# Kernel optimization log

Hardware: AMD Instinct MI355X
Metric: run time of the kernel (lower is better)

Reference implementation:

```python
import jax, jax.numpy as jnp
import numpy as np

SCALES = (2, 4, 8)  # primitive_scales, one per branch


def setup_inputs() -> dict:
    key = jax.random.key(0)
    k0, k1, k2, k3, k4 = jax.random.split(key, 5)
    B, C, H, W = 16, 256, 128, 128
    s = 1.0 / np.sqrt(C).astype(np.float32)
    return {
        "x": jax.random.normal(k0, (B, C, H, W), jnp.float32),
        "W_proto": jax.random.normal(k1, (3, C, C), jnp.float32) * s,
        "W_frame": jax.random.normal(k2, (3, C, C), jnp.float32) * s,
        "W_out": jax.random.normal(k3, (3, C, C), jnp.float32) * s,
        "W_fuse": jax.random.normal(k4, (C, 3 * C), jnp.float32) * (1.0 / np.sqrt(3 * C).astype(np.float32)),
    }


def _branch(x, Wp, Wf, Wo, P):
    # x: [B,C,H,W]; adaptive_avg_pool2d(x, (H, P)) with W % P == 0 == mean over equal bins along W
    B, C, H, W = x.shape
    proto = x.reshape(B, C, H, P, W // P).mean(axis=-1)        # [B,C,H,P]
    proto = jnp.einsum('oc,bchp->bohp', Wp, proto)             # proto_proj (1x1 conv)
    q = jnp.einsum('oc,bchw->bhwo', Wf, x)                     # frame_proj + permute -> [B,H,W,C]
    # att = q @ k, k = proto.permute(0,2,1,3) -> [B,H,C,P]
    att = jnp.einsum('bhwc,bchp->bhwp', q, proto) * (1.0 / jnp.sqrt(jnp.float32(C)))
    att = jax.nn.softmax(att, axis=-1)                         # [B,H,W,P]
    # v = proto.permute(0,2,3,1) -> [B,H,P,C]; msg = att @ v -> [B,H,W,C]
    msg = jnp.einsum('bhwp,bchp->bhwc', att, proto)
    return jnp.einsum('oc,bhwc->bohw', Wo, msg)                # out_proj -> [B,C,H,W]


def reference(x, W_proto, W_frame, W_out, W_fuse):
    outs = [_branch(x, W_proto[i], W_frame[i], W_out[i], SCALES[i]) for i in range(len(SCALES))]
    cat = jnp.concatenate(outs, axis=1)                        # [B, 3C, H, W]
    return jnp.einsum('oc,bchw->bohw', W_fuse, cat) + x
```

## Files before the change

kernel.cpp:

```cpp
#include <hip/hip_runtime.h>
#include <hip/hip_bf16.h>
#include <math.h>

#define CC   256
#define HW   (128*128)
#define MAT  (CC*CC)
#define NBH  2048
#define N0   4096
#define N1   8192
#define N2   16384

typedef __attribute__((ext_vector_type(8))) short bf16x8;
typedef __attribute__((ext_vector_type(4))) float f32x4;

__global__ __launch_bounds__(256) void k_mats1(
    const float* __restrict__ Wp, const float* __restrict__ Wf,
    const float* __restrict__ Wo, const float* __restrict__ Wfu,
    __hip_bfloat16* __restrict__ A, float* __restrict__ E)
{
    int idx = blockIdx.x;
    int t = threadIdx.x;
    if (idx < 3*CC) {
        int i = idx >> 8, c = idx & 255;
        const float* wf = Wf + (size_t)i*MAT;
        const float* wp = Wp + (size_t)i*MAT;
        float acc = 0.f;
        for (int o = 0; o < CC; ++o)
            acc += wf[o*CC + c] * wp[o*CC + t];
        A[(size_t)i*512*CC + (size_t)c*CC + t] = __float2bfloat16(acc);
    } else {
        idx -= 3*CC;
        int i = idx >> 8, o = idx & 255;
        const float* wo = Wo + (size_t)i*MAT;
        const float* wfu = Wfu + (size_t)o*(3*CC) + i*CC;
        float acc = 0.f;
        for (int c3 = 0; c3 < CC; ++c3)
            acc += wfu[c3] * wo[c3*CC + t];
        E[(size_t)i*MAT + (size_t)o*CC + t] = acc;
    }
}

__global__ __launch_bounds__(256) void k_mats2(
    const float* __restrict__ Wp, const float* __restrict__ E,
    __hip_bfloat16* __restrict__ A)
{
    int idx = blockIdx.x;
    int i = idx >> 8, o = idx & 255;
    int t = threadIdx.x;
    const float* e = E + (size_t)i*MAT + (size_t)o*CC;
    const float* wp = Wp + (size_t)i*MAT;
    float acc = 0.f;
    for (int c = 0; c < CC; ++c)
        acc += e[c] * wp[c*CC + t];
    A[(size_t)i*512*CC + (size_t)(256+o)*CC + t] = __float2bfloat16(acc);
}

__global__ __launch_bounds__(256) void k_poolA(
    const float* __restrict__ x, float* __restrict__ binsG)
{
    int bc = blockIdx.x;
    int t = threadIdx.x;
    const float4* xp = (const float4*)(x + (size_t)bc*HW) + t;
    __shared__ float bins[128][9];
    float4 v[16];
    #pragma unroll
    for (int i = 0; i < 16; ++i) v[i] = xp[i*256];
    int hb = t >> 5, bin = (t & 31) >> 2;
    #pragma unroll
    for (int i = 0; i < 16; ++i) {
        float s = v[i].x + v[i].y + v[i].z + v[i].w;
        s += __shfl_xor(s, 1);
        s += __shfl_xor(s, 2);
        if ((t & 3) == 0) bins[i*8 + hb][bin] = s;
    }
    __syncthreads();
    int h = t >> 1, b0 = (t & 1) * 4;
    float4 o;
    o.x = bins[h][b0+0]; o.y = bins[h][b0+1];
    o.z = bins[h][b0+2]; o.w = bins[h][b0+3];
    ((float4*)binsG)[(size_t)bc*256 + t] = o;
}

__global__ __launch_bounds__(256) void k_poolB(
    const float* __restrict__ binsG, __hip_bfloat16* __restrict__ Bt)
{
    int bh = blockIdx.x;
    int b = bh >> 7, h = bh & 127;
    int c = threadIdx.x;
    const float* g = binsG + (((size_t)b*256 + c)*128 + h)*8;
    float4 lo = *(const float4*)(g);
    float4 hi = *(const float4*)(g + 4);
    float b8[8] = {lo.x, lo.y, lo.z, lo.w, hi.x, hi.y, hi.z, hi.w};

    __hip_bfloat16* B0 = Bt;
    __hip_bfloat16* B1 = Bt + (size_t)N0*CC;
    __hip_bfloat16* B2 = Bt + (size_t)(N0+N1)*CC;
    B0[((size_t)bh*2 + 0)*CC + c] = __float2bfloat16((b8[0]+b8[1]+b8[2]+b8[3]) * (1.f/64.f));
    B0[((size_t)bh*2 + 1)*CC + c] = __float2bfloat16((b8[4]+b8[5]+b8[6]+b8[7]) * (1.f/64.f));
    #pragma unroll
    for (int j = 0; j < 4; ++j)
        B1[((size_t)bh*4 + j)*CC + c] = __float2bfloat16((b8[2*j]+b8[2*j+1]) * (1.f/32.f));
    #pragma unroll
    for (int j = 0; j < 8; ++j)
        B2[((size_t)bh*8 + j)*CC + c] = __float2bfloat16(b8[j] * (1.f/16.f));
}

__global__ __launch_bounds__(128) void k_gemm(
    const __hip_bfloat16* __restrict__ A,
    const __hip_bfloat16* __restrict__ Bt,
    float* __restrict__ Cc)
{
    int blk = blockIdx.x;
    int br, lb, LP, poff;
    if (blk < 256)      { br = 0; lb = blk;       LP = 1; poff = 0; }
    else if (blk < 768) { br = 1; lb = blk - 256; LP = 2; poff = 2; }
    else                { br = 2; lb = blk - 768; LP = 3; poff = 6; }
    size_t aoff  = (size_t)br*512*CC;
    size_t btoff = (br == 0) ? 0 : (br == 1 ? (size_t)N0*CC : (size_t)(N0+N1)*CC);
    const __hip_bfloat16* Ab = A  + aoff;
    const __hip_bfloat16* Bb = Bt + btoff;

    int rb = lb & 3, cb = lb >> 2;
    int wv = threadIdx.x >> 6, lane = threadIdx.x & 63;
    int row0 = rb*128 + wv*64;
    int col0 = cb*64;
    int lr = lane & 15, lk = (lane >> 4) * 8;

    f32x4 acc[4][4] = {};
    for (int kk = 0; kk < CC; kk += 32) {
        bf16x8 af[4], bfr[4];
        #pragma unroll
        for (int m = 0; m < 4; ++m)
            af[m] = *reinterpret_cast<const bf16x8*>(Ab + (size_t)(row0 + m*16 + lr)*CC + kk + lk);
        #pragma unroll
        for (int n = 0; n < 4; ++n)
            bfr[n] = *reinterpret_cast<const bf16x8*>(Bb + (size_t)(col0 + n*16 + lr)*CC + kk + lk);
        #pragma unroll
        for (int m = 0; m < 4; ++m)
            #pragma unroll
            for (int n = 0; n < 4; ++n)
                acc[m][n] = __builtin_amdgcn_mfma_f32_16x16x32_bf16(af[m], bfr[n], acc[m][n], 0, 0, 0);
    }

    int cr = (lane >> 4) * 4, ccol = lane & 15;
    int pm = (1 << LP) - 1;
    #pragma unroll
    for (int m = 0; m < 4; ++m) {
        #pragma unroll
        for (int n = 0; n < 4; ++n) {
            int colg = col0 + n*16 + ccol;
            int bh = colg >> LP, p = colg & pm;
            float* dst = Cc + (size_t)bh*8192 + poff + p;
            #pragma unroll
            for (int j = 0; j < 4; ++j) {
                int r = row0 + m*16 + cr + j;
                dst[r*16] = acc[m][n][j];
            }
        }
    }
}

template<int L>
__device__ __forceinline__ void softmax2(float2* a) {
    float mx = a[0].x, my = a[0].y;
    #pragma unroll
    for (int j = 1; j < L; ++j) { mx = fmaxf(mx, a[j].x); my = fmaxf(my, a[j].y); }
    float sx = 0.f, sy = 0.f;
    #pragma unroll
    for (int j = 0; j < L; ++j) {
        a[j].x = __expf(a[j].x - mx); sx += a[j].x;
        a[j].y = __expf(a[j].y - my); sy += a[j].y;
    }
    float rx = 1.f / sx, ry = 1.f / sy;
    #pragma unroll
    for (int j = 0; j < L; ++j) { a[j].x *= rx; a[j].y *= ry; }
}

__global__ __launch_bounds__(256) void k_main(
    const float* __restrict__ x, const float* __restrict__ Cc,
    float* __restrict__ out)
{
    int bh = blockIdx.x;
    int b = bh >> 7, h = bh & 127;
    int t = threadIdx.x;
    int lane = t & 63;
    int wv = __builtin_amdgcn_readfirstlane(t >> 6);
    const float* Cb = Cc + (size_t)bh * 8192;
    const float2* x2 = (const float2*)x + ((size_t)b*CC)*(HW/2) + h*64 + lane;
    float2*       o2 = (float2*)out     + ((size_t)b*CC)*(HW/2) + h*64 + lane;
    __shared__ float att_sx[2][64][15];
    __shared__ float att_sy[2][64][15];

    float2 att[14];
    #pragma unroll
    for (int p = 0; p < 14; ++p) att[p] = make_float2(0.f, 0.f);

    #pragma unroll 1
    for (int ccc = 0; ccc < 4; ++ccc) {
        float2 xv[16];
        #pragma unroll
        for (int j = 0; j < 16; ++j) {
            int c = ccc*64 + j*4 + wv;
            xv[j] = x2[c*(HW/2)];
        }
        #pragma unroll
        for (int j = 0; j < 16; ++j) {
            int c = ccc*64 + j*4 + wv;
            const float* mp = Cb + c*16;
            #pragma unroll
            for (int p = 0; p < 14; ++p) {
                att[p].x += xv[j].x * mp[p];
                att[p].y += xv[j].y * mp[p];
            }
        }
    }

    if (wv >= 2) {
        #pragma unroll
        for (int p = 0; p < 14; ++p) {
            att_sx[wv-2][lane][p] = att[p].x;
            att_sy[wv-2][lane][p] = att[p].y;
        }
    }
    __syncthreads();
    if (wv < 2) {
        #pragma unroll
        for (int p = 0; p < 14; ++p) {
            att[p].x += att_sx[wv][lane][p];
            att[p].y += att_sy[wv][lane][p];
        }
        if (wv == 1) {
            #pragma unroll
            for (int p = 0; p < 14; ++p) {
                att_sx[1][lane][p] = att[p].x;
                att_sy[1][lane][p] = att[p].y;
            }
        }
    }
    __syncthreads();
    if (wv == 0) {
        #pragma unroll
        for (int p = 0; p < 14; ++p) {
            att[p].x = (att[p].x + att_sx[1][lane][p]) * 0.0625f;
            att[p].y = (att[p].y + att_sy[1][lane][p]) * 0.0625f;
        }
        softmax2<2>(att + 0);
        softmax2<4>(att + 2);
        softmax2<8>(att + 6);
        #pragma unroll
        for (int p = 0; p < 14; ++p) {
            att_sx[0][lane][p] = att[p].x;
            att_sy[0][lane][p] = att[p].y;
        }
    }
    __syncthreads();
    #pragma unroll
    for (int p = 0; p < 14; ++p) {
        att[p].x = att_sx[0][lane][p];
        att[p].y = att_sy[0][lane][p];
    }

    #pragma unroll 1
    for (int ooo = 0; ooo < 4; ++ooo) {
        float2 xv[16];
        #pragma unroll
        for (int j = 0; j < 16; ++j) {
            int o = ooo*64 + j*4 + wv;
            xv[j] = x2[o*(HW/2)];
        }
        #pragma unroll
        for (int j = 0; j < 16; ++j) {
            int o = ooo*64 + j*4 + wv;
            const float* vp = Cb + (256 + o)*16;
            float2 acc = xv[j];
            #pragma unroll
            for (int p = 0; p < 14; ++p) {
                acc.x += att[p].x * vp[p];
                acc.y += att[p].y * vp[p];
            }
            o2[o*(HW/2)] = acc;
        }
    }
}

extern "C" void kernel_launch(void* const* d_in, const int* in_sizes, int n_in,
                              void* d_out, int out_size, void* d_ws, size_t ws_size,
                              hipStream_t stream)
{
    (void)in_sizes; (void)n_in; (void)out_size; (void)ws_size;
    const float* x   = (const float*)d_in[0];
    const float* Wp  = (const float*)d_in[1];
    const float* Wf  = (const float*)d_in[2];
    const float* Wo  = (const float*)d_in[3];
    const float* Wfu = (const float*)d_in[4];
    float* out = (float*)d_out;

    char* wsb = (char*)d_ws;
    float*          E     = (float*)wsb;
    __hip_bfloat16* A     = (__hip_bfloat16*)(wsb + 786432);
    __hip_bfloat16* Bt    = (__hip_bfloat16*)(wsb + 1572864);
    float*          Cc    = (float*)(wsb + 16252928);
    float*          binsG = Cc;

    k_mats1<<<dim3(6*CC),  dim3(256), 0, stream>>>(Wp, Wf, Wo, Wfu, A, E);
    k_mats2<<<dim3(3*CC),  dim3(256), 0, stream>>>(Wp, E, A);
    k_poolA<<<dim3(4096),  dim3(256), 0, stream>>>(x, binsG);
    k_poolB<<<dim3(NBH),   dim3(256), 0, stream>>>(binsG, Bt);
    k_gemm <<<dim3(1792),  dim3(128), 0, stream>>>(A, Bt, Cc);
    k_main <<<dim3(NBH),   dim3(256), 0, stream>>>(x, Cc, out);
}
```

Baseline: 347.8 us.

## Cache x slice in registers across both k_main passes; split pooling blocks in half

```diff
diff --git a/kernel.cpp b/kernel.cpp
--- a/kernel.cpp
+++ b/kernel.cpp
@@ -58,27 +58,30 @@
 __global__ __launch_bounds__(256) void k_poolA(
     const float* __restrict__ x, float* __restrict__ binsG)
 {
-    int bc = blockIdx.x;
+    int blk = blockIdx.x;
+    int bc = blk >> 1, half = blk & 1;
     int t = threadIdx.x;
-    const float4* xp = (const float4*)(x + (size_t)bc*HW) + t;
-    __shared__ float bins[128][9];
-    float4 v[16];
-    #pragma unroll
-    for (int i = 0; i < 16; ++i) v[i] = xp[i*256];
+    const float4* xp = (const float4*)(x + (size_t)bc*HW + half*8192) + t;
+    __shared__ float bins[64][9];
+    float4 v[8];
+    #pragma unroll
+    for (int i = 0; i < 8; ++i) v[i] = xp[i*256];
     int hb = t >> 5, bin = (t & 31) >> 2;
     #pragma unroll
-    for (int i = 0; i < 16; ++i) {
+    for (int i = 0; i < 8; ++i) {
         float s = v[i].x + v[i].y + v[i].z + v[i].w;
         s += __shfl_xor(s, 1);
         s += __shfl_xor(s, 2);
         if ((t & 3) == 0) bins[i*8 + hb][bin] = s;
     }
     __syncthreads();
-    int h = t >> 1, b0 = (t & 1) * 4;
-    float4 o;
-    o.x = bins[h][b0+0]; o.y = bins[h][b0+1];
-    o.z = bins[h][b0+2]; o.w = bins[h][b0+3];
-    ((float4*)binsG)[(size_t)bc*256 + t] = o;
+    if (t < 128) {
+        int h = t >> 1, b0 = (t & 1) * 4;
+        float4 o;
+        o.x = bins[h][b0+0]; o.y = bins[h][b0+1];
+        o.z = bins[h][b0+2]; o.w = bins[h][b0+3];
+        ((float4*)binsG)[(size_t)bc*256 + half*128 + t] = o;
+    }
 }
 
 __global__ __launch_bounds__(256) void k_poolB(
@@ -176,7 +179,7 @@
     for (int j = 0; j < L; ++j) { a[j].x *= rx; a[j].y *= ry; }
 }
 
-__global__ __launch_bounds__(256) void k_main(
+__global__ __launch_bounds__(256, 2) void k_main(
     const float* __restrict__ x, const float* __restrict__ Cc,
     float* __restrict__ out)
 {
@@ -191,27 +194,23 @@
     __shared__ float att_sx[2][64][15];
     __shared__ float att_sy[2][64][15];
 
+    float2 xc[64];
+    #pragma unroll
+    for (int j = 0; j < 64; ++j)
+        xc[j] = x2[(size_t)(j*4 + wv)*(HW/2)];
+
     float2 att[14];
     #pragma unroll
     for (int p = 0; p < 14; ++p) att[p] = make_float2(0.f, 0.f);
 
-    #pragma unroll 1
-    for (int ccc = 0; ccc < 4; ++ccc) {
-        float2 xv[16];
-        #pragma unroll
-        for (int j = 0; j < 16; ++j) {
-            int c = ccc*64 + j*4 + wv;
-            xv[j] = x2[c*(HW/2)];
-        }
-        #pragma unroll
-        for (int j = 0; j < 16; ++j) {
-            int c = ccc*64 + j*4 + wv;
-            const float* mp = Cb + c*16;
-            #pragma unroll
-            for (int p = 0; p < 14; ++p) {
-                att[p].x += xv[j].x * mp[p];
-                att[p].y += xv[j].y * mp[p];
-            }
+    #pragma unroll
+    for (int j = 0; j < 64; ++j) {
+        int c = j*4 + wv;
+        const float* mp = Cb + c*16;
+        #pragma unroll
+        for (int p = 0; p < 14; ++p) {
+            att[p].x += xc[j].x * mp[p];
+            att[p].y += xc[j].y * mp[p];
         }
     }
 
@@ -260,26 +259,17 @@
         att[p].y = att_sy[0][lane][p];
     }
 
-    #pragma unroll 1
-    for (int ooo = 0; ooo < 4; ++ooo) {
-        float2 xv[16];
-        #pragma unroll
-        for (int j = 0; j < 16; ++j) {
-            int o = ooo*64 + j*4 + wv;
-            xv[j] = x2[o*(HW/2)];
-        }
-        #pragma unroll
-        for (int j = 0; j < 16; ++j) {
-            int o = ooo*64 + j*4 + wv;
-            const float* vp = Cb + (256 + o)*16;
-            float2 acc = xv[j];
-            #pragma unroll
-            for (int p = 0; p < 14; ++p) {
-                acc.x += att[p].x * vp[p];
-                acc.y += att[p].y * vp[p];
-            }
-            o2[o*(HW/2)] = acc;
-        }
+    #pragma unroll
+    for (int j = 0; j < 64; ++j) {
+        int o = j*4 + wv;
+        const float* vp = Cb + (256 + o)*16;
+        float2 acc = xc[j];
+        #pragma unroll
+        for (int p = 0; p < 14; ++p) {
+            acc.x += att[p].x * vp[p];
+            acc.y += att[p].y * vp[p];
+        }
+        o2[(size_t)o*(HW/2)] = acc;
     }
 }
 
@@ -304,7 +294,7 @@
 
     k_mats1<<<dim3(6*CC),  dim3(256), 0, stream>>>(Wp, Wf, Wo, Wfu, A, E);
     k_mats2<<<dim3(3*CC),  dim3(256), 0, stream>>>(Wp, E, A);
-    k_poolA<<<dim3(4096),  dim3(256), 0, stream>>>(x, binsG);
+    k_poolA<<<dim3(8192),  dim3(256), 0, stream>>>(x, binsG);
     k_poolB<<<dim3(NBH),   dim3(256), 0, stream>>>(binsG, Bt);
     k_gemm <<<dim3(1792),  dim3(128), 0, stream>>>(A, Bt, Cc);
     k_main <<<dim3(NBH),   dim3(256), 0, stream>>>(x, Cc, out);
```

Result: slower. 491.7 us (+41.4%).

## Stage x through LDS with async triple buffering and store per-row matrices in bf16

Applied to the files above, without the earlier changes.

```diff
diff --git a/kernel.cpp b/kernel.cpp
--- a/kernel.cpp
+++ b/kernel.cpp
@@ -1,6 +1,7 @@
 #include <hip/hip_runtime.h>
 #include <hip/hip_bf16.h>
 #include <math.h>
+#include <stdint.h>
 
 #define CC   256
 #define HW   (128*128)
@@ -12,6 +13,8 @@
 
 typedef __attribute__((ext_vector_type(8))) short bf16x8;
 typedef __attribute__((ext_vector_type(4))) float f32x4;
+typedef __attribute__((address_space(3))) uint32_t lds_u32_t;
+typedef __attribute__((address_space(1))) const uint32_t glb_u32_t;
 
 __global__ __launch_bounds__(256) void k_mats1(
     const float* __restrict__ Wp, const float* __restrict__ Wf,
@@ -55,7 +58,7 @@
     A[(size_t)i*512*CC + (size_t)(256+o)*CC + t] = __float2bfloat16(acc);
 }
 
-__global__ __launch_bounds__(256) void k_poolA(
+__global__ __launch_bounds__(256, 4) void k_poolA(
     const float* __restrict__ x, float* __restrict__ binsG)
 {
     int bc = blockIdx.x;
@@ -108,7 +111,7 @@
 __global__ __launch_bounds__(128) void k_gemm(
     const __hip_bfloat16* __restrict__ A,
     const __hip_bfloat16* __restrict__ Bt,
-    float* __restrict__ Cc)
+    __hip_bfloat16* __restrict__ Cc)
 {
     int blk = blockIdx.x;
     int br, lb, LP, poff;
@@ -150,11 +153,11 @@
         for (int n = 0; n < 4; ++n) {
             int colg = col0 + n*16 + ccol;
             int bh = colg >> LP, p = colg & pm;
-            float* dst = Cc + (size_t)bh*8192 + poff + p;
+            __hip_bfloat16* dst = Cc + (size_t)bh*8192 + poff + p;
             #pragma unroll
             for (int j = 0; j < 4; ++j) {
                 int r = row0 + m*16 + cr + j;
-                dst[r*16] = acc[m][n][j];
+                dst[r*16] = __float2bfloat16(acc[m][n][j]);
             }
         }
     }
@@ -176,8 +179,8 @@
     for (int j = 0; j < L; ++j) { a[j].x *= rx; a[j].y *= ry; }
 }
 
-__global__ __launch_bounds__(256) void k_main(
-    const float* __restrict__ x, const float* __restrict__ Cc,
+__global__ __launch_bounds__(256, 4) void k_main(
+    const float* __restrict__ x, const __hip_bfloat16* __restrict__ Cc,
     float* __restrict__ out)
 {
     int bh = blockIdx.x;
@@ -185,9 +188,11 @@
     int t = threadIdx.x;
     int lane = t & 63;
     int wv = __builtin_amdgcn_readfirstlane(t >> 6);
-    const float* Cb = Cc + (size_t)bh * 8192;
-    const float2* x2 = (const float2*)x + ((size_t)b*CC)*(HW/2) + h*64 + lane;
-    float2*       o2 = (float2*)out     + ((size_t)b*CC)*(HW/2) + h*64 + lane;
+    const uint32_t* Cb = (const uint32_t*)(Cc + (size_t)bh*8192);
+    const float* xg = x  + ((size_t)b*CC)*HW + h*128;
+    float*       og = out + ((size_t)b*CC)*HW + h*128;
+
+    __shared__ float xbuf[3][32*128];
     __shared__ float att_sx[2][64][15];
     __shared__ float att_sy[2][64][15];
 
@@ -195,90 +200,123 @@
     #pragma unroll
     for (int p = 0; p < 14; ++p) att[p] = make_float2(0.f, 0.f);
 
+    auto STAGE = [&](int tt) {
+        int cb = (tt & 7) * 32;
+        float* bufp = xbuf[tt % 3];
+        #pragma unroll
+        for (int q = 0; q < 4; ++q) {
+            int c0 = cb + wv*8 + q*2;
+            const float* gp = xg + (size_t)(c0 + (lane >> 5))*HW + (lane & 31)*4;
+            float* lp = &bufp[(wv*8 + q*2)*128];
+            __builtin_amdgcn_global_load_lds((glb_u32_t*)gp, (lds_u32_t*)lp, 16, 0, 0);
+        }
+    };
+
+    STAGE(0);
+    STAGE(1);
+
     #pragma unroll 1
-    for (int ccc = 0; ccc < 4; ++ccc) {
-        float2 xv[16];
-        #pragma unroll
-        for (int j = 0; j < 16; ++j) {
-            int c = ccc*64 + j*4 + wv;
-            xv[j] = x2[c*(HW/2)];
-        }
-        #pragma unroll
-        for (int j = 0; j < 16; ++j) {
-            int c = ccc*64 + j*4 + wv;
-            const float* mp = Cb + c*16;
+    for (int tt = 0; tt < 16; ++tt) {
+        if (tt < 15) asm volatile("s_waitcnt vmcnt(4)" ::: "memory");
+        else         asm volatile("s_waitcnt vmcnt(0)" ::: "memory");
+        __builtin_amdgcn_s_barrier();
+        __builtin_amdgcn_sched_barrier(0);
+
+        if (tt == 8) {
+            if (wv >= 2) {
+                #pragma unroll
+                for (int p = 0; p < 14; ++p) {
+                    att_sx[wv-2][lane][p] = att[p].x;
+                    att_sy[wv-2][lane][p] = att[p].y;
+                }
+            }
+            asm volatile("s_waitcnt lgkmcnt(0)" ::: "memory");
+            __builtin_amdgcn_s_barrier();
+            __builtin_amdgcn_sched_barrier(0);
+            if (wv < 2) {
+                #pragma unroll
+                for (int p = 0; p < 14; ++p) {
+                    att[p].x += att_sx[wv][lane][p];
+                    att[p].y += att_sy[wv][lane][p];
+                }
+                if (wv == 1) {
+                    #pragma unroll
+                    for (int p = 0; p < 14; ++p) {
+                        att_sx[1][lane][p] = att[p].x;
+                        att_sy[1][lane][p] = att[p].y;
+                    }
+                }
+            }
+            asm volatile("s_waitcnt lgkmcnt(0)" ::: "memory");
+            __builtin_amdgcn_s_barrier();
+            __builtin_amdgcn_sched_barrier(0);
+            if (wv == 0) {
+                #pragma unroll
+                for (int p = 0; p < 14; ++p) {
+                    att[p].x = (att[p].x + att_sx[1][lane][p]) * 0.0625f;
+                    att[p].y = (att[p].y + att_sy[1][lane][p]) * 0.0625f;
+                }
+                softmax2<2>(att + 0);
+                softmax2<4>(att + 2);
+                softmax2<8>(att + 6);
+                #pragma unroll
+                for (int p = 0; p < 14; ++p) {
+                    att_sx[0][lane][p] = att[p].x;
+                    att_sy[0][lane][p] = att[p].y;
+                }
+            }
+            asm volatile("s_waitcnt lgkmcnt(0)" ::: "memory");
+            __builtin_amdgcn_s_barrier();
+            __builtin_amdgcn_sched_barrier(0);
             #pragma unroll
             for (int p = 0; p < 14; ++p) {
-                att[p].x += xv[j].x * mp[p];
-                att[p].y += xv[j].y * mp[p];
+                att[p].x = att_sx[0][lane][p];
+                att[p].y = att_sy[0][lane][p];
             }
         }
-    }
-
-    if (wv >= 2) {
-        #pragma unroll
-        for (int p = 0; p < 14; ++p) {
-            att_sx[wv-2][lane][p] = att[p].x;
-            att_sy[wv-2][lane][p] = att[p].y;
-        }
-    }
-    __syncthreads();
-    if (wv < 2) {
-        #pragma unroll
-        for (int p = 0; p < 14; ++p) {
-            att[p].x += att_sx[wv][lane][p];
-            att[p].y += att_sy[wv][lane][p];
-        }
-        if (wv == 1) {
+
+        if (tt + 2 < 16) STAGE(tt + 2);
+
+        {
+            int cb = (tt & 7) * 32;
+            bool passB = (tt >= 8);
+            const float* xb = &xbuf[tt % 3][(wv*8)*128];
+            int crow = (passB ? 256 : 0) + cb + wv*8;
+            const uint32_t* wr = Cb + (size_t)crow*8;
             #pragma unroll
-            for (int p = 0; p < 14; ++p) {
-                att_sx[1][lane][p] = att[p].x;
-                att_sy[1][lane][p] = att[p].y;
-            }
-        }
-    }
-    __syncthreads();
-    if (wv == 0) {
-        #pragma unroll
-        for (int p = 0; p < 14; ++p) {
-            att[p].x = (att[p].x + att_sx[1][lane][p]) * 0.0625f;
-            att[p].y = (att[p].y + att_sy[1][lane][p]) * 0.0625f;
-        }
-        softmax2<2>(att + 0);
-        softmax2<4>(att + 2);
-        softmax2<8>(att + 6);
-        #pragma unroll
-        for (int p = 0; p < 14; ++p) {
-            att_sx[0][lane][p] = att[p].x;
-            att_sy[0][lane][p] = att[p].y;
-        }
-    }
-    __syncthreads();
-    #pragma unroll
-    for (int p = 0; p < 14; ++p) {
-        att[p].x = att_sx[0][lane][p];
-        att[p].y = att_sy[0][lane][p];
-    }
-
-    #pragma unroll 1
-    for (int ooo = 0; ooo < 4; ++ooo) {
-        float2 xv[16];
-        #pragma unroll
-        for (int j = 0; j < 16; ++j) {
-            int o = ooo*64 + j*4 + wv;
-            xv[j] = x2[o*(HW/2)];
-        }
-        #pragma unroll
-        for (int j = 0; j < 16; ++j) {
-            int o = ooo*64 + j*4 + wv;
-            const float* vp = Cb + (256 + o)*16;
-            float2 acc = xv[j];
-            #pragma unroll
-            for (int p = 0; p < 14; ++p) {
-                acc.x += att[p].x * vp[p];
-                acc.y += att[p].y * vp[p];
-            }
-            o2[o*(HW/2)] = acc;
+            for (int half = 0; half < 2; ++half) {
+                uint32_t u[4][7];
+                #pragma unroll
+                for (int q = 0; q < 4; ++q)
+                    #pragma unroll
+                    for (int j = 0; j < 7; ++j)
+                        u[q][j] = wr[(half*4 + q)*8 + j];
+                #pragma unroll
+                for (int q = 0; q < 4; ++q) {
+                    int qq = half*4 + q;
+                    float2 xv = *(const float2*)&xb[qq*128 + lane*2];
+                    if (!passB) {
+                        #pragma unroll
+                        for (int j = 0; j < 7; ++j) {
+                            float mlo = __uint_as_float(u[q][j] << 16);
+                            float mhi = __uint_as_float(u[q][j] & 0xFFFF0000u);
+                            att[2*j].x   += xv.x * mlo;  att[2*j].y   += xv.y * mlo;
+                            att[2*j+1].x += xv.x * mhi;  att[2*j+1].y += xv.y * mhi;
+                        }
+                    } else {
+                        float2 acc = xv;
+                        #pragma unroll
+                        for (int j = 0; j < 7; ++j) {
+                            float vlo = __uint_as_float(u[q][j] << 16);
+                            float vhi = __uint_as_float(u[q][j] & 0xFFFF0000u);
+                            acc.x += att[2*j].x * vlo;   acc.y += att[2*j].y * vlo;
+                            acc.x += att[2*j+1].x * vhi; acc.y += att[2*j+1].y * vhi;
+                        }
+                        int o = cb + wv*8 + qq;
+                        *(float2*)&og[(size_t)o*HW + lane*2] = acc;
+                    }
+                }
+            }
         }
     }
 }
@@ -299,8 +337,8 @@
     float*          E     = (float*)wsb;
     __hip_bfloat16* A     = (__hip_bfloat16*)(wsb + 786432);
     __hip_bfloat16* Bt    = (__hip_bfloat16*)(wsb + 1572864);
-    float*          Cc    = (float*)(wsb + 16252928);
-    float*          binsG = Cc;
+    __hip_bfloat16* Cc    = (__hip_bfloat16*)(wsb + 16252928);
+    float*          binsG = (float*)(wsb + 16252928);
 
     k_mats1<<<dim3(6*CC),  dim3(256), 0, stream>>>(Wp, Wf, Wo, Wfu, A, E);
     k_mats2<<<dim3(3*CC),  dim3(256), 0, stream>>>(Wp, E, A);
```

Measured after the change: 334.1 us. 4.0% less time.

## Store per-row coefficient table in bf16 and double-buffer x loads in k_main

Applied to the files above, without the earlier changes.

```diff
diff --git a/kernel.cpp b/kernel.cpp
--- a/kernel.cpp
+++ b/kernel.cpp
@@ -1,6 +1,7 @@
 #include <hip/hip_runtime.h>
 #include <hip/hip_bf16.h>
 #include <math.h>
+#include <stdint.h>
 
 #define CC   256
 #define HW   (128*128)
@@ -55,7 +56,7 @@
     A[(size_t)i*512*CC + (size_t)(256+o)*CC + t] = __float2bfloat16(acc);
 }
 
-__global__ __launch_bounds__(256) void k_poolA(
+__global__ __launch_bounds__(256, 4) void k_poolA(
     const float* __restrict__ x, float* __restrict__ binsG)
 {
     int bc = blockIdx.x;
@@ -108,7 +109,7 @@
 __global__ __launch_bounds__(128) void k_gemm(
     const __hip_bfloat16* __restrict__ A,
     const __hip_bfloat16* __restrict__ Bt,
-    float* __restrict__ Cc)
+    __hip_bfloat16* __restrict__ Cc)
 {
     int blk = blockIdx.x;
     int br, lb, LP, poff;
@@ -150,11 +151,11 @@
         for (int n = 0; n < 4; ++n) {
             int colg = col0 + n*16 + ccol;
             int bh = colg >> LP, p = colg & pm;
-            float* dst = Cc + (size_t)bh*8192 + poff + p;
+            __hip_bfloat16* dst = Cc + (size_t)bh*8192 + poff + p;
             #pragma unroll
             for (int j = 0; j < 4; ++j) {
                 int r = row0 + m*16 + cr + j;
-                dst[r*16] = acc[m][n][j];
+                dst[r*16] = __float2bfloat16(acc[m][n][j]);
             }
         }
     }
@@ -176,8 +177,8 @@
     for (int j = 0; j < L; ++j) { a[j].x *= rx; a[j].y *= ry; }
 }
 
-__global__ __launch_bounds__(256) void k_main(
-    const float* __restrict__ x, const float* __restrict__ Cc,
+__global__ __launch_bounds__(256, 4) void k_main(
+    const float* __restrict__ x, const __hip_bfloat16* __restrict__ Cc,
     float* __restrict__ out)
 {
     int bh = blockIdx.x;
@@ -185,7 +186,7 @@
     int t = threadIdx.x;
     int lane = t & 63;
     int wv = __builtin_amdgcn_readfirstlane(t >> 6);
-    const float* Cb = Cc + (size_t)bh * 8192;
+    const uint32_t* Cb = (const uint32_t*)(Cc + (size_t)bh*8192);
     const float2* x2 = (const float2*)x + ((size_t)b*CC)*(HW/2) + h*64 + lane;
     float2*       o2 = (float2*)out     + ((size_t)b*CC)*(HW/2) + h*64 + lane;
     __shared__ float att_sx[2][64][15];
@@ -195,25 +196,59 @@
     #pragma unroll
     for (int p = 0; p < 14; ++p) att[p] = make_float2(0.f, 0.f);
 
-    #pragma unroll 1
-    for (int ccc = 0; ccc < 4; ++ccc) {
-        float2 xv[16];
-        #pragma unroll
-        for (int j = 0; j < 16; ++j) {
-            int c = ccc*64 + j*4 + wv;
-            xv[j] = x2[c*(HW/2)];
-        }
-        #pragma unroll
-        for (int j = 0; j < 16; ++j) {
-            int c = ccc*64 + j*4 + wv;
-            const float* mp = Cb + c*16;
-            #pragma unroll
-            for (int p = 0; p < 14; ++p) {
-                att[p].x += xv[j].x * mp[p];
-                att[p].y += xv[j].y * mp[p];
-            }
-        }
-    }
+    float2 xa[8], xb[8];
+
+    #define CH(cc, j) (((cc)*8 + (j))*4 + wv)
+
+    #define LOADB(buf, cc)                                                  \
+        _Pragma("unroll")                                                   \
+        for (int j = 0; j < 8; ++j)                                         \
+            buf[j] = x2[(size_t)CH(cc, j) * (HW/2)];
+
+    #define CONS_A(buf, cc)                                                 \
+        _Pragma("unroll")                                                   \
+        for (int j = 0; j < 8; ++j) {                                       \
+            int c = CH(cc, j);                                              \
+            const uint32_t* wr = Cb + (size_t)c*8;                          \
+            float2 xv = buf[j];                                             \
+            _Pragma("unroll")                                               \
+            for (int p = 0; p < 7; ++p) {                                   \
+                uint32_t u = wr[p];                                         \
+                float mlo = __uint_as_float(u << 16);                       \
+                float mhi = __uint_as_float(u & 0xFFFF0000u);               \
+                att[2*p].x   += xv.x * mlo;  att[2*p].y   += xv.y * mlo;    \
+                att[2*p+1].x += xv.x * mhi;  att[2*p+1].y += xv.y * mhi;    \
+            }                                                               \
+        }
+
+    #define CONS_B(buf, cc)                                                 \
+        _Pragma("unroll")                                                   \
+        for (int j = 0; j < 8; ++j) {                                       \
+            int c = CH(cc, j);                                              \
+            const uint32_t* wr = Cb + (size_t)(256 + c)*8;                  \
+            float2 acc = buf[j];                                            \
+            _Pragma("unroll")                                               \
+            for (int p = 0; p < 7; ++p) {                                   \
+                uint32_t u = wr[p];                                         \
+                float vlo = __uint_as_float(u << 16);                       \
+                float vhi = __uint_as_float(u & 0xFFFF0000u);               \
+                acc.x += att[2*p].x * vlo;   acc.y += att[2*p].y * vlo;     \
+                acc.x += att[2*p+1].x * vhi; acc.y += att[2*p+1].y * vhi;   \
+            }                                                               \
+            o2[(size_t)c * (HW/2)] = acc;                                   \
+        }
+
+    #define SB __builtin_amdgcn_sched_barrier(0)
+
+    LOADB(xa, 0); LOADB(xb, 1); SB;
+    CONS_A(xa, 0); LOADB(xa, 2); SB;
+    CONS_A(xb, 1); LOADB(xb, 3); SB;
+    CONS_A(xa, 2); LOADB(xa, 4); SB;
+    CONS_A(xb, 3); LOADB(xb, 5); SB;
+    CONS_A(xa, 4); LOADB(xa, 6); SB;
+    CONS_A(xb, 5); LOADB(xb, 7); SB;
+    CONS_A(xa, 6); SB;
+    CONS_A(xb, 7);
 
     if (wv >= 2) {
         #pragma unroll
@@ -260,27 +295,21 @@
         att[p].y = att_sy[0][lane][p];
     }
 
-    #pragma unroll 1
-    for (int ooo = 0; ooo < 4; ++ooo) {
-        float2 xv[16];
-        #pragma unroll
-        for (int j = 0; j < 16; ++j) {
-            int o = ooo*64 + j*4 + wv;
-            xv[j] = x2[o*(HW/2)];
-        }
-        #pragma unroll
-        for (int j = 0; j < 16; ++j) {
-            int o = ooo*64 + j*4 + wv;
-            const float* vp = Cb + (256 + o)*16;
-            float2 acc = xv[j];
-            #pragma unroll
-            for (int p = 0; p < 14; ++p) {
-                acc.x += att[p].x * vp[p];
-                acc.y += att[p].y * vp[p];
-            }
-            o2[o*(HW/2)] = acc;
-        }
-    }
+    LOADB(xa, 0); LOADB(xb, 1); SB;
+    CONS_B(xa, 0); LOADB(xa, 2); SB;
+    CONS_B(xb, 1); LOADB(xb, 3); SB;
+    CONS_B(xa, 2); LOADB(xa, 4); SB;
+    CONS_B(xb, 3); LOADB(xb, 5); SB;
+    CONS_B(xa, 4); LOADB(xa, 6); SB;
+    CONS_B(xb, 5); LOADB(xb, 7); SB;
+    CONS_B(xa, 6); SB;
+    CONS_B(xb, 7);
+
+    #undef CH
+    #undef LOADB
+    #undef CONS_A
+    #undef CONS_B
+    #undef SB
 }
 
 extern "C" void kernel_launch(void* const* d_in, const int* in_sizes, int n_in,
@@ -299,8 +328,8 @@
     float*          E     = (float*)wsb;
     __hip_bfloat16* A     = (__hip_bfloat16*)(wsb + 786432);
     __hip_bfloat16* Bt    = (__hip_bfloat16*)(wsb + 1572864);
-    float*          Cc    = (float*)(wsb + 16252928);
-    float*          binsG = Cc;
+    __hip_bfloat16* Cc    = (__hip_bfloat16*)(wsb + 16252928);
+    float*          binsG = (float*)(wsb + 16252928);
 
     k_mats1<<<dim3(6*CC),  dim3(256), 0, stream>>>(Wp, Wf, Wo, Wfu, A, E);
     k_mats2<<<dim3(3*CC),  dim3(256), 0, stream>>>(Wp, E, A);
```

New measurement: 466.6 us. 1.34x slower.
